# Performance work log

Hardware: AMD Instinct MI355X
Metric: run time of the kernel (lower is better)

Reference implementation:

```python
import jax, jax.numpy as jnp
import numpy as np

NHEADS = 16
HEAD_DIM = 64
HIDDEN = 1024
QKV = NHEADS * HEAD_DIM  # 1024
SCALING = HEAD_DIM ** -0.5


def setup_inputs() -> dict:
    key = jax.random.key(0)
    k1, k2, k3, k4, k5 = jax.random.split(key, 5)
    B, S = 2, 2048
    hidden_states = jax.random.normal(k1, (B, S, HIDDEN), dtype=jnp.float32)
    # nn.Linear weights: stored [out, in]; kaiming-uniform-ish init scale
    w_qkv = jax.random.normal(k2, (3 * QKV, HIDDEN), dtype=jnp.float32) * (HIDDEN ** -0.5)
    b_qkv = jax.random.normal(k3, (3 * QKV,), dtype=jnp.float32) * 0.01
    w_o = jax.random.normal(k4, (HIDDEN, QKV), dtype=jnp.float32) * (QKV ** -0.5)
    b_o = jax.random.normal(k5, (HIDDEN,), dtype=jnp.float32) * 0.01
    return {"hidden_states": hidden_states, "w_qkv": w_qkv, "b_qkv": b_qkv,
            "w_o": w_o, "b_o": b_o}


def reference(hidden_states, w_qkv, b_qkv, w_o, b_o):
    B, S, _ = hidden_states.shape
    # qkv projection: x @ W^T + b  (torch nn.Linear convention)
    qkv = jnp.einsum('bsh,oh->bso', hidden_states, w_qkv) + b_qkv  # [B,S,3*QKV]
    xq, xk, xv = jnp.split(qkv, 3, axis=-1)
    # [B,S,H,D] -> [B,H,S,D]
    q = xq.reshape(B, S, NHEADS, HEAD_DIM).transpose(0, 2, 1, 3)
    k = xk.reshape(B, S, NHEADS, HEAD_DIM).transpose(0, 2, 1, 3)
    v = xv.reshape(B, S, NHEADS, HEAD_DIM).transpose(0, 2, 1, 3)
    scores = jnp.einsum('bhqd,bhkd->bhqk', q, k) * SCALING
    # dropout is identity in eval mode; mask is None in this config
    probs = jax.nn.softmax(scores.astype(jnp.float32), axis=-1).astype(q.dtype)
    out = jnp.einsum('bhqk,bhkd->bhqd', probs, v)  # [B,H,S,D]
    out = out.transpose(0, 2, 1, 3).reshape(B, S, QKV)
    return jnp.einsum('bsq,oq->bso', out, w_o) + b_o
```

## Files before the change

### kernel.cpp

```cpp
#include <hip/hip_runtime.h>

#define SEQ     2048
#define MROWS   4096
#define HID     1024
#define QKV3    3072
#define NH      16
#define HD      64
#define QSCALE  0.18033688f

typedef unsigned short u16;
typedef unsigned int   u32;
typedef __attribute__((ext_vector_type(8)))  short  bf16x8;
typedef __attribute__((ext_vector_type(4)))  float  floatx4;
typedef __attribute__((ext_vector_type(16))) float  floatx16;
typedef __attribute__((ext_vector_type(4)))  unsigned int u32x4;

__device__ __forceinline__ u16 f2bf(float f) {
    u32 u = __builtin_bit_cast(u32, f);
    u += 0x7fffu + ((u >> 16) & 1u);
    return (u16)(u >> 16);
}

#if __has_builtin(__builtin_amdgcn_exp2f)
__device__ __forceinline__ float fast_exp2(float x) { return __builtin_amdgcn_exp2f(x); }
#else
__device__ __forceinline__ float fast_exp2(float x) { return exp2f(x); }
#endif

#if __has_builtin(__builtin_amdgcn_cvt_pk_bf16_f32)
__device__ __forceinline__ u32 pack_bf(float a, float b) {
    auto r = __builtin_amdgcn_cvt_pk_bf16_f32(a, b);
    return __builtin_bit_cast(u32, r);
}
#else
__device__ __forceinline__ u32 pack_bf(float a, float b) {
    u32 ua = __builtin_bit_cast(u32, a) + 0x8000u;
    u32 ub = __builtin_bit_cast(u32, b) + 0x8000u;
    return __builtin_amdgcn_perm(ub, ua, 0x07060302u);
}
#endif

__device__ __forceinline__ void plane_swap(u32 &x, u32 &y) {
#if __has_builtin(__builtin_amdgcn_permlane32_swap)
    typedef __attribute__((ext_vector_type(2))) unsigned int u32x2;
    u32x2 r = __builtin_amdgcn_permlane32_swap(x, y, false, false);
    x = r[0]; y = r[1];
#else
    asm volatile("v_permlane32_swap_b32 %0, %1" : "+v"(x), "+v"(y));
#endif
}

__device__ __forceinline__ void async_cp16(const void* g, void* l) {
    __builtin_amdgcn_global_load_lds(
        (const __attribute__((address_space(1))) unsigned int*)g,
        (__attribute__((address_space(3))) unsigned int*)l, 16, 0, 0);
}

#define N4_X   (MROWS * HID / 4)
#define N4_WQ  (QKV3 * HID / 4)
#define N4_WO  (HID * HID / 4)
__global__ void cvt_all(const float* __restrict__ x, const float* __restrict__ wq,
                        const float* __restrict__ wo, u16* __restrict__ xb,
                        u16* __restrict__ wqb, u16* __restrict__ wob) {
    int i = blockIdx.x * blockDim.x + threadIdx.x;
    const float* src; u16* dst; int k;
    if (i < N4_X)                { src = x;  dst = xb;  k = i; }
    else if (i < N4_X + N4_WQ)   { src = wq; dst = wqb; k = i - N4_X; }
    else                         { src = wo; dst = wob; k = i - N4_X - N4_WQ; }
    float4 v = ((const float4*)src)[k];
    uint2 o = {pack_bf(v.x, v.y), pack_bf(v.z, v.w)};
    ((uint2*)dst)[k] = o;
}

template <int MODE, int NT>
__global__ __launch_bounds__(256)
void gemm_bf16_nt(const u16* __restrict__ A, const u16* __restrict__ B,
                  const float* __restrict__ bias, float* __restrict__ Cout,
                  int M, int N, int K,
                  u16* __restrict__ q_ws, u16* __restrict__ k_ws,
                  u16* __restrict__ vt_ws) {
    constexpr int WN = NT / 2;
    constexpr int NJ = WN / 16;
    __shared__ u16 As[2][128 * 32];
    __shared__ u16 Bs[2][NT * 32];
    const int t  = (int)threadIdx.x;
    const int w  = t >> 6, l = t & 63;
    const int wr = w >> 1, wc = w & 1;
    const int m0 = (int)blockIdx.y * 128, n0 = (int)blockIdx.x * NT;
    const int lrow = l >> 2;
    const int lseg = ((l & 3) ^ ((l >> 3) & 3)) * 8;
    const int fm = l & 15, fq = l >> 4;
    const int fseg = (fq ^ ((fm >> 1) & 3)) * 8;

    auto stage = [&](int k0, int bb) {
#pragma unroll
        for (int rep = 0; rep < 2; ++rep) {
            const int chunk = w + rep * 4;
            const int row   = chunk * 16 + lrow;
            async_cp16(A + (size_t)(m0 + row) * K + k0 + lseg, &As[bb][chunk * 512]);
            if (NT == 128 || rep == 0)
                async_cp16(B + (size_t)(n0 + row) * K + k0 + lseg, &Bs[bb][chunk * 512]);
        }
    };

    floatx4 acc[4][NJ];
#pragma unroll
    for (int i = 0; i < 4; ++i)
#pragma unroll
        for (int j = 0; j < NJ; ++j) acc[i][j] = (floatx4)(0.f);

    const int T = K >> 5;
    stage(0, 0);
    for (int tt = 0; tt < T; ++tt) {
        const int cur = tt & 1;
        __syncthreads();
        if (tt + 1 < T) stage((tt + 1) << 5, cur ^ 1);
        bf16x8 af[4], bf[NJ];
#pragma unroll
        for (int i = 0; i < 4; ++i)
            af[i] = *(const bf16x8*)&As[cur][(wr * 64 + i * 16 + fm) * 32 + fseg];
#pragma unroll
        for (int j = 0; j < NJ; ++j)
            bf[j] = *(const bf16x8*)&Bs[cur][(wc * WN + j * 16 + fm) * 32 + fseg];
#pragma unroll
        for (int i = 0; i < 4; ++i)
#pragma unroll
            for (int j = 0; j < NJ; ++j)
                acc[i][j] = __builtin_amdgcn_mfma_f32_16x16x32_bf16(
                    af[i], bf[j], acc[i][j], 0, 0, 0);
    }

#pragma unroll
    for (int j = 0; j < NJ; ++j) {
        const int col = n0 + wc * WN + j * 16 + fm;
        const float bv = bias[col];
        const int region = col >> 10;
        const int hh = (col >> 6) & 15, d = col & 63;
#pragma unroll
        for (int i = 0; i < 4; ++i) {
            const int row0 = m0 + wr * 64 + i * 16 + fq * 4;
            if (MODE == 0) {
#pragma unroll
                for (int r = 0; r < 4; ++r)
                    Cout[(size_t)(row0 + r) * N + col] = acc[i][j][r] + bv;
            } else if (region < 2) {
                u16* __restrict__ dst = (region == 0) ? q_ws : k_ws;
                const float sc = (region == 0) ? QSCALE : 1.0f;
#pragma unroll
                for (int r = 0; r < 4; ++r) {
                    const int row = row0 + r;
                    const int b = row >> 11, s = row & 2047;
                    dst[((size_t)(b * NH + hh) * SEQ + s) * HD + d] =
                        f2bf((acc[i][j][r] + bv) * sc);
                }
            } else {
                const int b = row0 >> 11, s0 = row0 & 2047;
                uint2 o = {pack_bf(acc[i][j][0] + bv, acc[i][j][1] + bv),
                           pack_bf(acc[i][j][2] + bv, acc[i][j][3] + bv)};
                *(uint2*)&vt_ws[((size_t)(b * NH + hh) * HD + d) * SEQ + s0] = o;
            }
        }
    }
}

__global__ __launch_bounds__(256, 2)
void attn_mfma(const u16* __restrict__ qw, const u16* __restrict__ kw,
               const u16* __restrict__ vtw, u16* __restrict__ attn) {
    __shared__ u16 Ks [2][64 * 64];
    __shared__ u16 Vts[2][64 * 64];

    const int bh   = (int)blockIdx.x;
    const int qblk = (int)blockIdx.y * 128;
    const int t = (int)threadIdx.x;
    const int w = t >> 6, l = t & 63;
    const int ql = l & 31, h = l >> 5;
    const int srow = l >> 3, sseg = l & 7;
    const size_t headSD = (size_t)bh * SEQ * HD;
    const size_t headDS = (size_t)bh * HD * SEQ;

    auto stage = [&](int kt, int bb) {
#pragma unroll
        for (int rep = 0; rep < 2; ++rep) {
            const int chunk = w * 2 + rep;
            async_cp16(kw + headSD + (size_t)(kt * 64 + chunk * 8 + srow) * HD
                           + ((sseg ^ srow) * 8), &Ks[bb][chunk * 512]);
            async_cp16(vtw + headDS + (size_t)(chunk * 8 + srow) * SEQ + kt * 64
                           + ((sseg ^ srow) * 8), &Vts[bb][chunk * 512]);
        }
    };

    bf16x8 qa[4];
#pragma unroll
    for (int ks = 0; ks < 4; ++ks)
        qa[ks] = *(const bf16x8*)(qw + headSD
            + (size_t)(qblk + w * 32 + ql) * HD + ks * 16 + h * 8);

    floatx16 oacc[2];
#pragma unroll
    for (int dt = 0; dt < 2; ++dt) oacc[dt] = (floatx16)(0.f);
    float psum = 0.f;

    stage(0, 0);
    for (int kt = 0; kt < SEQ / 64; ++kt) {
        const int cur = kt & 1;
        __syncthreads();
        if (kt + 1 < SEQ / 64) stage(kt + 1, cur ^ 1);

        floatx16 sacc[2];
        sacc[0] = (floatx16)(0.f); sacc[1] = (floatx16)(0.f);
        __builtin_amdgcn_s_setprio(1);
#pragma unroll
        for (int ks = 0; ks < 4; ++ks) {
            const int seg = (ks * 2 + h) ^ (ql & 7);
#pragma unroll
            for (int t2 = 0; t2 < 2; ++t2) {
                bf16x8 ka = *(const bf16x8*)&Ks[cur][(t2 * 32 + ql) * 64 + seg * 8];
                sacc[t2] = __builtin_amdgcn_mfma_f32_32x32x16_bf16(
                    ka, qa[ks], sacc[t2], 0, 0, 0);
            }
        }
        __builtin_amdgcn_s_setprio(0);

#pragma unroll
        for (int t2 = 0; t2 < 2; ++t2) {
            u32 aw[8];
#pragma unroll
            for (int i = 0; i < 8; ++i) {
                const float p0 = fast_exp2(sacc[t2][2 * i]);
                const float p1 = fast_exp2(sacc[t2][2 * i + 1]);
                psum += p0 + p1;
                aw[i] = pack_bf(p0, p1);
            }
            plane_swap(aw[0], aw[2]); plane_swap(aw[1], aw[3]);
            plane_swap(aw[4], aw[6]); plane_swap(aw[5], aw[7]);

            __builtin_amdgcn_s_setprio(1);
#pragma unroll
            for (int ks2 = 0; ks2 < 2; ++ks2) {
                u32x4 pw = {aw[4 * ks2 + 0], aw[4 * ks2 + 1],
                            aw[4 * ks2 + 2], aw[4 * ks2 + 3]};
                bf16x8 pb = __builtin_bit_cast(bf16x8, pw);
                const int seg = (t2 * 4 + ks2 * 2 + h) ^ (ql & 7);
#pragma unroll
                for (int dt = 0; dt < 2; ++dt) {
                    bf16x8 va = *(const bf16x8*)&Vts[cur][(dt * 32 + ql) * 64 + seg * 8];
                    oacc[dt] = __builtin_amdgcn_mfma_f32_32x32x16_bf16(
                        va, pb, oacc[dt], 0, 0, 0);
                }
            }
            __builtin_amdgcn_s_setprio(0);
        }
    }

    psum += __shfl_xor(psum, 32);
    const float inv = 1.0f / psum;

    const int b = bh >> 4, head = bh & 15;
    u16* __restrict__ orow =
        attn + (size_t)(b * SEQ + qblk + w * 32 + ql) * HID + head * HD;
#pragma unroll
    for (int dt = 0; dt < 2; ++dt) {
#pragma unroll
        for (int g = 0; g < 4; ++g) {
            uint2 o = {pack_bf(oacc[dt][g * 4 + 0] * inv, oacc[dt][g * 4 + 1] * inv),
                       pack_bf(oacc[dt][g * 4 + 2] * inv, oacc[dt][g * 4 + 3] * inv)};
            *(uint2*)&orow[dt * 32 + g * 8 + h * 4] = o;
        }
    }
}

extern "C" void kernel_launch(void* const* d_in, const int* in_sizes, int n_in,
                              void* d_out, int out_size, void* d_ws, size_t ws_size,
                              hipStream_t stream) {
    const float* x     = (const float*)d_in[0];
    const float* w_qkv = (const float*)d_in[1];
    const float* b_qkv = (const float*)d_in[2];
    const float* w_o   = (const float*)d_in[3];
    const float* b_o   = (const float*)d_in[4];
    float* outp = (float*)d_out;

    u16* xb    = (u16*)d_ws;
    u16* wqkvb = xb    + (size_t)MROWS * HID;
    u16* wob   = wqkvb + (size_t)QKV3 * HID;
    u16* q_ws  = wob   + (size_t)HID * HID;
    u16* k_ws  = q_ws  + (size_t)MROWS * HID;
    u16* vt_ws = k_ws  + (size_t)MROWS * HID;
    u16* attnb = vt_ws + (size_t)MROWS * HID;

    const int blk = 256;
    cvt_all<<<(N4_X + N4_WQ + N4_WO) / blk, blk, 0, stream>>>(
        x, w_qkv, w_o, xb, wqkvb, wob);

    gemm_bf16_nt<1, 128><<<dim3(QKV3 / 128, MROWS / 128), blk, 0, stream>>>(
        xb, wqkvb, b_qkv, nullptr, MROWS, QKV3, HID, q_ws, k_ws, vt_ws);

    attn_mfma<<<dim3(NH * 2, SEQ / 128), 256, 0, stream>>>(q_ws, k_ws, vt_ws, attnb);

    gemm_bf16_nt<0, 64><<<dim3(HID / 64, MROWS / 128), blk, 0, stream>>>(
        attnb, wob, b_o, outp, MROWS, HID, HID, nullptr, nullptr, nullptr);
}
```

Before: 187.4 us.

## Process two 64-key tiles per attention iteration to halve barriers

The attention kernel now stages and processes two 64-key K/V tiles per loop iteration. This halves the number of __syncthreads barriers and exposes more independent QK^T MFMAs before the softmax exp work. It also drops the s_setprio hints, splits the probability sum into two accumulators, and zeroes the score accumulator on the first MFMA. Shared memory doubles to 64 KB per block and register pressure rises, which may hurt occupancy at launch_bounds(256,2).

```diff
diff --git a/kernel.cpp b/kernel.cpp
--- a/kernel.cpp
+++ b/kernel.cpp
@@ -115,19 +115,19 @@
         const int cur = tt & 1;
         __syncthreads();
         if (tt + 1 < T) stage((tt + 1) << 5, cur ^ 1);
-        bf16x8 af[4], bf[NJ];
+        bf16x8 af[4], bfr[NJ];
 #pragma unroll
         for (int i = 0; i < 4; ++i)
             af[i] = *(const bf16x8*)&As[cur][(wr * 64 + i * 16 + fm) * 32 + fseg];
 #pragma unroll
         for (int j = 0; j < NJ; ++j)
-            bf[j] = *(const bf16x8*)&Bs[cur][(wc * WN + j * 16 + fm) * 32 + fseg];
+            bfr[j] = *(const bf16x8*)&Bs[cur][(wc * WN + j * 16 + fm) * 32 + fseg];
 #pragma unroll
         for (int i = 0; i < 4; ++i)
 #pragma unroll
             for (int j = 0; j < NJ; ++j)
                 acc[i][j] = __builtin_amdgcn_mfma_f32_16x16x32_bf16(
-                    af[i], bf[j], acc[i][j], 0, 0, 0);
+                    af[i], bfr[j], acc[i][j], 0, 0, 0);
     }
 
 #pragma unroll
@@ -166,8 +166,8 @@
 __global__ __launch_bounds__(256, 2)
 void attn_mfma(const u16* __restrict__ qw, const u16* __restrict__ kw,
                const u16* __restrict__ vtw, u16* __restrict__ attn) {
-    __shared__ u16 Ks [2][64 * 64];
-    __shared__ u16 Vts[2][64 * 64];
+    __shared__ u16 Ks [2][2][64 * 64];
+    __shared__ u16 Vts[2][2][64 * 64];
 
     const int bh   = (int)blockIdx.x;
     const int qblk = (int)blockIdx.y * 128;
@@ -178,14 +178,18 @@
     const size_t headSD = (size_t)bh * SEQ * HD;
     const size_t headDS = (size_t)bh * HD * SEQ;
 
-    auto stage = [&](int kt, int bb) {
-#pragma unroll
-        for (int rep = 0; rep < 2; ++rep) {
-            const int chunk = w * 2 + rep;
-            async_cp16(kw + headSD + (size_t)(kt * 64 + chunk * 8 + srow) * HD
-                           + ((sseg ^ srow) * 8), &Ks[bb][chunk * 512]);
-            async_cp16(vtw + headDS + (size_t)(chunk * 8 + srow) * SEQ + kt * 64
-                           + ((sseg ^ srow) * 8), &Vts[bb][chunk * 512]);
+    auto stage = [&](int it, int bb) {
+#pragma unroll
+        for (int half = 0; half < 2; ++half) {
+            const int kt = it * 2 + half;
+#pragma unroll
+            for (int rep = 0; rep < 2; ++rep) {
+                const int chunk = w * 2 + rep;
+                async_cp16(kw + headSD + (size_t)(kt * 64 + chunk * 8 + srow) * HD
+                               + ((sseg ^ srow) * 8), &Ks[bb][half][chunk * 512]);
+                async_cp16(vtw + headDS + (size_t)(chunk * 8 + srow) * SEQ + kt * 64
+                               + ((sseg ^ srow) * 8), &Vts[bb][half][chunk * 512]);
+            }
         }
     };
 
@@ -195,63 +199,65 @@
         qa[ks] = *(const bf16x8*)(qw + headSD
             + (size_t)(qblk + w * 32 + ql) * HD + ks * 16 + h * 8);
 
+    const floatx16 z16 = (floatx16)(0.f);
     floatx16 oacc[2];
-#pragma unroll
-    for (int dt = 0; dt < 2; ++dt) oacc[dt] = (floatx16)(0.f);
-    float psum = 0.f;
+    oacc[0] = z16; oacc[1] = z16;
+    float2 psum2 = {0.f, 0.f};
 
     stage(0, 0);
-    for (int kt = 0; kt < SEQ / 64; ++kt) {
-        const int cur = kt & 1;
+    for (int it = 0; it < SEQ / 128; ++it) {
+        const int cur = it & 1;
         __syncthreads();
-        if (kt + 1 < SEQ / 64) stage(kt + 1, cur ^ 1);
-
-        floatx16 sacc[2];
-        sacc[0] = (floatx16)(0.f); sacc[1] = (floatx16)(0.f);
-        __builtin_amdgcn_s_setprio(1);
-#pragma unroll
-        for (int ks = 0; ks < 4; ++ks) {
-            const int seg = (ks * 2 + h) ^ (ql & 7);
-#pragma unroll
-            for (int t2 = 0; t2 < 2; ++t2) {
-                bf16x8 ka = *(const bf16x8*)&Ks[cur][(t2 * 32 + ql) * 64 + seg * 8];
-                sacc[t2] = __builtin_amdgcn_mfma_f32_32x32x16_bf16(
-                    ka, qa[ks], sacc[t2], 0, 0, 0);
-            }
-        }
-        __builtin_amdgcn_s_setprio(0);
-
-#pragma unroll
-        for (int t2 = 0; t2 < 2; ++t2) {
-            u32 aw[8];
-#pragma unroll
-            for (int i = 0; i < 8; ++i) {
-                const float p0 = fast_exp2(sacc[t2][2 * i]);
-                const float p1 = fast_exp2(sacc[t2][2 * i + 1]);
-                psum += p0 + p1;
-                aw[i] = pack_bf(p0, p1);
-            }
-            plane_swap(aw[0], aw[2]); plane_swap(aw[1], aw[3]);
-            plane_swap(aw[4], aw[6]); plane_swap(aw[5], aw[7]);
-
-            __builtin_amdgcn_s_setprio(1);
-#pragma unroll
-            for (int ks2 = 0; ks2 < 2; ++ks2) {
-                u32x4 pw = {aw[4 * ks2 + 0], aw[4 * ks2 + 1],
-                            aw[4 * ks2 + 2], aw[4 * ks2 + 3]};
-                bf16x8 pb = __builtin_bit_cast(bf16x8, pw);
-                const int seg = (t2 * 4 + ks2 * 2 + h) ^ (ql & 7);
-#pragma unroll
-                for (int dt = 0; dt < 2; ++dt) {
-                    bf16x8 va = *(const bf16x8*)&Vts[cur][(dt * 32 + ql) * 64 + seg * 8];
-                    oacc[dt] = __builtin_amdgcn_mfma_f32_32x32x16_bf16(
-                        va, pb, oacc[dt], 0, 0, 0);
+        if (it + 1 < SEQ / 128) stage(it + 1, cur ^ 1);
+
+        floatx16 sacc[2][2];
+#pragma unroll
+        for (int half = 0; half < 2; ++half) {
+#pragma unroll
+            for (int ks = 0; ks < 4; ++ks) {
+                const int seg = ((ks * 2 + h) ^ (ql & 7)) * 8;
+#pragma unroll
+                for (int t2 = 0; t2 < 2; ++t2) {
+                    bf16x8 ka = *(const bf16x8*)&Ks[cur][half][(t2 * 32 + ql) * 64 + seg];
+                    sacc[half][t2] = __builtin_amdgcn_mfma_f32_32x32x16_bf16(
+                        ka, qa[ks], (ks == 0) ? z16 : sacc[half][t2], 0, 0, 0);
                 }
             }
-            __builtin_amdgcn_s_setprio(0);
+        }
+
+#pragma unroll
+        for (int half = 0; half < 2; ++half) {
+#pragma unroll
+            for (int t2 = 0; t2 < 2; ++t2) {
+                u32 aw[8];
+#pragma unroll
+                for (int i = 0; i < 8; ++i) {
+                    const float p0 = fast_exp2(sacc[half][t2][2 * i]);
+                    const float p1 = fast_exp2(sacc[half][t2][2 * i + 1]);
+                    psum2 += float2{p0, p1};
+                    aw[i] = pack_bf(p0, p1);
+                }
+                plane_swap(aw[0], aw[2]); plane_swap(aw[1], aw[3]);
+                plane_swap(aw[4], aw[6]); plane_swap(aw[5], aw[7]);
+
+#pragma unroll
+                for (int ks2 = 0; ks2 < 2; ++ks2) {
+                    u32x4 pw = {aw[4 * ks2 + 0], aw[4 * ks2 + 1],
+                                aw[4 * ks2 + 2], aw[4 * ks2 + 3]};
+                    bf16x8 pb = __builtin_bit_cast(bf16x8, pw);
+                    const int seg = ((t2 * 4 + ks2 * 2 + h) ^ (ql & 7)) * 8;
+#pragma unroll
+                    for (int dt = 0; dt < 2; ++dt) {
+                        bf16x8 va = *(const bf16x8*)&Vts[cur][half][(dt * 32 + ql) * 64 + seg];
+                        oacc[dt] = __builtin_amdgcn_mfma_f32_32x32x16_bf16(
+                            va, pb, oacc[dt], 0, 0, 0);
+                    }
+                }
+            }
         }
     }
 
+    float psum = psum2.x + psum2.y;
     psum += __shfl_xor(psum, 32);
     const float inv = 1.0f / psum;
 
```

Measured after the change: 183.3 us. -2.2%, faster.
